# Kernel tuning notes

Measured on AMD Instinct MI355X. Metric: run time of the kernel, lower is better.

The kernel has to match this reference:

```python
import jax, jax.numpy as jnp
import numpy as np

K = 3   # spatial_kernel_size
M = 5   # memory_size


def setup_inputs() -> dict:
    key = jax.random.key(0)
    ks = jax.random.split(key, 16)
    C = 64
    B, H, D, W = 2, 24, 24, 24
    s = 0.05
    n = jax.random.normal
    return {
        "x": n(ks[0], (B, C, H, D, W), jnp.float32),
        "prev_memory": jnp.zeros((B, C), jnp.float32),
        "Wq": n(ks[1], (C, C), jnp.float32) * s,
        "bq": n(ks[2], (C,), jnp.float32) * s,
        "Wk": n(ks[3], (C, C), jnp.float32) * s,
        "bk": n(ks[4], (C,), jnp.float32) * s,
        "Wv": n(ks[5], (C, C), jnp.float32) * s,
        "bv": n(ks[6], (C,), jnp.float32) * s,
        "mem_key": n(ks[7], (C, M), jnp.float32),
        "mem_value": n(ks[8], (C, M), jnp.float32),
        "Wg": n(ks[9], (C, 2 * C), jnp.float32) * s,
        "bg": n(ks[10], (C,), jnp.float32) * s,
        "W_ih": n(ks[11], (3 * C, C), jnp.float32) * s,
        "W_hh": n(ks[12], (3 * C, C), jnp.float32) * s,
        "b_ih": n(ks[13], (3 * C,), jnp.float32) * s,
        "b_hh": n(ks[14], (3 * C,), jnp.float32) * s,
    }


def _patches(x, k):
    # x: (B,C,H,D,W) -> (B,C,k^3,H,D,W) local neighborhoods (zero-padded)
    B, C, H, D, W = x.shape
    p = k // 2
    xp = jnp.pad(x, ((0, 0), (0, 0), (p, p), (p, p), (p, p)))
    sl = [xp[:, :, i:i + H, j:j + D, l:l + W]
          for i in range(k) for j in range(k) for l in range(k)]
    return jnp.stack(sl, axis=2)


def reference(x, prev_memory, Wq, bq, Wk, bk, Wv, bv, mem_key, mem_value,
              Wg, bg, W_ih, W_hh, b_ih, b_hh):
    B, C, H, D, W = x.shape
    N = H * D * W
    xf = x.reshape(B, C, N)
    pf = _patches(x, K).reshape(B, C, K ** 3, N)

    # 1x1x1 conv projections (pure channel mixes)
    q = jnp.einsum('oc,bcn->bon', Wq, xf) + bq[None, :, None]            # (B,C,N)
    k_sp = jnp.einsum('oc,bcmn->bomn', Wk, pf) + bk[None, :, None, None]  # (B,C,27,N)
    v_sp = jnp.einsum('oc,bcmn->bomn', Wv, pf) + bv[None, :, None, None]

    # memory tokens broadcast over all spatial locations
    k_mem = jnp.broadcast_to(mem_key[None, :, :, None], (B, C, M, N))
    v_mem = jnp.broadcast_to(mem_value[None, :, :, None], (B, C, M, N))
    kk = jnp.concatenate([k_mem, k_sp], axis=2)   # (B,C,M+27,N)
    vv = jnp.concatenate([v_mem, v_sp], axis=2)

    # per-channel scalar attention over memory+neighborhood axis
    attn = jax.nn.softmax(q[:, :, None, :] * kk / jnp.sqrt(jnp.float32(C)), axis=2)
    out = jnp.sum(attn * vv, axis=2).reshape(B, C, H, D, W)

    # sigmoid gate over concat([x, out])
    gin = jnp.concatenate([xf, out.reshape(B, C, N)], axis=1)  # (B,2C,N)
    gate = jax.nn.sigmoid(jnp.einsum('oc,bcn->bon', Wg, gin)
                          + bg[None, :, None]).reshape(B, C, H, D, W)
    out = gate * out + (1.0 - gate) * x

    # GRU memory update on spatially pooled features (torch GRUCell math)
    mu = out.mean(axis=(2, 3, 4))                 # (B,C)
    gi = mu @ W_ih.T + b_ih
    gh = prev_memory @ W_hh.T + b_hh
    ir, iz, ii = jnp.split(gi, 3, axis=1)
    hr, hz, hn = jnp.split(gh, 3, axis=1)
    r = jax.nn.sigmoid(ir + hr)
    z = jax.nn.sigmoid(iz + hz)
    ng = jnp.tanh(ii + r * hn)
    new_memory = (1.0 - z) * ng + z * prev_memory
    return out, new_memory
```

## Files before the change

### kernel.cpp

```cpp
#include <hip/hip_runtime.h>
#include <math.h>

#define NPOS 13824
#define CDIM 64
#define BTCH 2
#define LOG2E 1.4426950408889634f

__global__ __launch_bounds__(256) void qkvg_kernel(
    const float* __restrict__ x,
    const float* __restrict__ Wq, const float* __restrict__ bq,
    const float* __restrict__ Wk, const float* __restrict__ bk,
    const float* __restrict__ Wv, const float* __restrict__ bv,
    const float* __restrict__ Wg,
    float* __restrict__ Qb, float* __restrict__ Kb, float* __restrict__ Vb,
    float* __restrict__ GXb, float* __restrict__ XT, float* __restrict__ pool)
{
  __shared__ __align__(16) float wqt[64*68];
  __shared__ __align__(16) float wkt[64*68];
  __shared__ __align__(16) float wvt[64*68];
  __shared__ __align__(16) float wgt[64*68];
  const int t  = threadIdx.x;
  const int bi = blockIdx.x;
  const int b  = bi / 216;
  const int n0 = (bi - b*216) * 64;
  if (bi == 0 && t < 128) pool[t] = 0.0f;

  #pragma unroll
  for (int k = 0; k < 16; ++k) {
    int idx = t + k*256;
    int lo = idx & 63, hi = idx >> 6;
    wqt[lo*68 + hi] = Wq[idx];
    wkt[lo*68 + hi] = Wk[idx];
    wvt[lo*68 + hi] = Wv[idx];
    wgt[lo*68 + hi] = Wg[hi*128 + lo];
  }
  __syncthreads();

  const int c0  = (t & 15) * 4;
  const int nn0 = (t >> 4) * 4;
  const float* xbase = x + (size_t)(b*64)*NPOS + n0 + nn0;
  float aq[4][4] = {}; float ak[4][4] = {}; float av[4][4] = {}; float ag[4][4] = {};
  #pragma unroll 4
  for (int cp = 0; cp < 64; ++cp) {
    const float4 xv4 = *(const float4*)(xbase + (size_t)cp*NPOS);
    const float4 q4  = *(const float4*)&wqt[cp*68 + c0];
    const float4 k4  = *(const float4*)&wkt[cp*68 + c0];
    const float4 v4  = *(const float4*)&wvt[cp*68 + c0];
    const float4 g4  = *(const float4*)&wgt[cp*68 + c0];
    const float xa[4] = {xv4.x, xv4.y, xv4.z, xv4.w};
    const float qa[4] = {q4.x, q4.y, q4.z, q4.w};
    const float ka[4] = {k4.x, k4.y, k4.z, k4.w};
    const float va[4] = {v4.x, v4.y, v4.z, v4.w};
    const float ga[4] = {g4.x, g4.y, g4.z, g4.w};
    #pragma unroll
    for (int ci = 0; ci < 4; ++ci)
      #pragma unroll
      for (int ni = 0; ni < 4; ++ni) {
        aq[ci][ni] = fmaf(qa[ci], xa[ni], aq[ci][ni]);
        ak[ci][ni] = fmaf(ka[ci], xa[ni], ak[ci][ni]);
        av[ci][ni] = fmaf(va[ci], xa[ni], av[ci][ni]);
        ag[ci][ni] = fmaf(ga[ci], xa[ni], ag[ci][ni]);
      }
  }
  const float4 bq4 = *(const float4*)&bq[c0];
  const float4 bk4 = *(const float4*)&bk[c0];
  const float4 bv4 = *(const float4*)&bv[c0];
  #pragma unroll
  for (int ni = 0; ni < 4; ++ni) {
    const int p = b*NPOS + n0 + nn0 + ni;
    float4 o;
    o = make_float4(aq[0][ni]+bq4.x, aq[1][ni]+bq4.y, aq[2][ni]+bq4.z, aq[3][ni]+bq4.w);
    *(float4*)&Qb[p*64 + c0] = o;
    o = make_float4(ak[0][ni]+bk4.x, ak[1][ni]+bk4.y, ak[2][ni]+bk4.z, ak[3][ni]+bk4.w);
    *(float4*)&Kb[p*64 + c0] = o;
    o = make_float4(av[0][ni]+bv4.x, av[1][ni]+bv4.y, av[2][ni]+bv4.z, av[3][ni]+bv4.w);
    *(float4*)&Vb[p*64 + c0] = o;
    o = make_float4(ag[0][ni], ag[1][ni], ag[2][ni], ag[3][ni]);
    *(float4*)&GXb[p*64 + c0] = o;
  }
  float4 xr[4];
  #pragma unroll
  for (int e = 0; e < 4; ++e)
    xr[e] = *(const float4*)(x + (size_t)(b*64 + c0 + e)*NPOS + n0 + nn0);
  const float xre[4][4] = {{xr[0].x,xr[0].y,xr[0].z,xr[0].w},
                           {xr[1].x,xr[1].y,xr[1].z,xr[1].w},
                           {xr[2].x,xr[2].y,xr[2].z,xr[2].w},
                           {xr[3].x,xr[3].y,xr[3].z,xr[3].w}};
  #pragma unroll
  for (int ni = 0; ni < 4; ++ni) {
    const int p = b*NPOS + n0 + nn0 + ni;
    *(float4*)&XT[p*64 + c0] = make_float4(xre[0][ni], xre[1][ni], xre[2][ni], xre[3][ni]);
  }
}

__global__ __launch_bounds__(256) void attn_kernel(
    float* __restrict__ QOT,
    const float* __restrict__ Kb, const float* __restrict__ Vb,
    const float* __restrict__ GXb, const float* __restrict__ XT,
    const float* __restrict__ bk, const float* __restrict__ bv,
    const float* __restrict__ memk, const float* __restrict__ memv,
    const float* __restrict__ Wg, const float* __restrict__ bg)
{
  __shared__ __align__(16) float smem[16000];
  __shared__ __align__(16) float als[256];
  const int t = threadIdx.x;
  const int c = t & 63;
  const int w = t >> 6;

  #pragma unroll
  for (int k = 0; k < 16; ++k) {
    int u = t + k*256;
    int cp = u >> 6, j = u & 63;
    smem[j*65 + cp] = Wg[cp*128 + 64 + j];
  }
  __syncthreads();
  float wg2reg[64];
  #pragma unroll
  for (int j = 0; j < 64; ++j) wg2reg[j] = smem[j*65 + c];
  float mk[5], mv[5];
  #pragma unroll
  for (int m = 0; m < 5; ++m) { mk[m] = memk[c*5 + m]; mv[m] = memv[c*5 + m]; }
  const float bg_c = bg[c];
  __syncthreads();

  const int bi = blockIdx.x;
  const int b  = bi >> 9;
  const int tb = bi & 511;
  const int h0 = (tb >> 6) * 3;
  const int d0 = ((tb >> 3) & 7) * 3;
  const int w0 = (tb & 7) * 3;
  const int bN = b * NPOS;

  for (int u = t; u < 125*16; u += 256) {
    int pos = u >> 4, q4 = u & 15;
    int ph = pos / 25, pr = pos - ph*25;
    int pd = pr / 5,  pw = pr - pd*5;
    int hh = h0 - 1 + ph, dd = d0 - 1 + pd, ww = w0 - 1 + pw;
    bool inb = ((unsigned)hh < 24u) && ((unsigned)dd < 24u) && ((unsigned)ww < 24u);
    float4 kf, vf;
    if (inb) {
      const size_t off = ((size_t)(bN + hh*576 + dd*24 + ww))*64 + q4*4;
      kf = *(const float4*)(Kb + off);
      vf = *(const float4*)(Vb + off);
    } else {
      kf = ((const float4*)bk)[q4];
      vf = ((const float4*)bv)[q4];
    }
    *(float4*)&smem[pos*64 + q4*4]        = kf;
    *(float4*)&smem[8000 + pos*64 + q4*4] = vf;
  }
  __syncthreads();

  for (int li = w; li < 27; li += 4) {
    const int lh = li / 9, lr = li - lh*9;
    const int ld = lr / 3, lw = lr - ld*3;
    const int p  = bN + (h0+lh)*576 + (d0+ld)*24 + (w0+lw);
    const int hb = (lh*25 + ld*5 + lw)*64 + c;

    const float q2 = QOT[p*64 + c] * (0.125f * LOG2E);
    float lg[32];
    #pragma unroll
    for (int m = 0; m < 5; ++m) lg[m] = q2 * mk[m];
    #pragma unroll
    for (int i = 0; i < 3; ++i)
      #pragma unroll
      for (int j = 0; j < 3; ++j)
        #pragma unroll
        for (int l = 0; l < 3; ++l)
          lg[5 + i*9 + j*3 + l] = q2 * smem[hb + (i*25 + j*5 + l)*64];

    float m0 = lg[0], m1 = lg[1], m2 = lg[2], m3 = lg[3];
    #pragma unroll
    for (int s4 = 4; s4 < 32; s4 += 4) {
      m0 = fmaxf(m0, lg[s4]);   m1 = fmaxf(m1, lg[s4+1]);
      m2 = fmaxf(m2, lg[s4+2]); m3 = fmaxf(m3, lg[s4+3]);
    }
    const float maxv = fmaxf(fmaxf(m0, m1), fmaxf(m2, m3));

    float s0 = 0.f, s1 = 0.f, o0 = 0.f, o1 = 0.f;
    #pragma unroll
    for (int m = 0; m < 5; ++m) {
      float pf = exp2f(lg[m] - maxv);
      if (m & 1) { s1 += pf; o1 = fmaf(pf, mv[m], o1); }
      else       { s0 += pf; o0 = fmaf(pf, mv[m], o0); }
    }
    #pragma unroll
    for (int i = 0; i < 3; ++i)
      #pragma unroll
      for (int j = 0; j < 3; ++j)
        #pragma unroll
        for (int l = 0; l < 3; ++l) {
          int s4 = i*9 + j*3 + l;
          float val = smem[8000 + hb + (i*25 + j*5 + l)*64];
          float pf = exp2f(lg[5 + s4] - maxv);
          if (s4 & 1) { s1 += pf; o1 = fmaf(pf, val, o1); }
          else        { s0 += pf; o0 = fmaf(pf, val, o0); }
        }
    const float att = (o0 + o1) * __builtin_amdgcn_rcpf(s0 + s1);

    als[w*64 + c] = att;
    float g0 = GXb[p*64 + c] + bg_c, g1 = 0.f, g2 = 0.f, g3 = 0.f;
    #pragma unroll
    for (int j4 = 0; j4 < 16; ++j4) {
      const float4 a4 = *(const float4*)&als[w*64 + j4*4];
      g0 = fmaf(wg2reg[j4*4+0], a4.x, g0);
      g1 = fmaf(wg2reg[j4*4+1], a4.y, g1);
      g2 = fmaf(wg2reg[j4*4+2], a4.z, g2);
      g3 = fmaf(wg2reg[j4*4+3], a4.w, g3);
    }
    const float gl   = (g0 + g1) + (g2 + g3);
    const float gate = __builtin_amdgcn_rcpf(1.0f + exp2f(-LOG2E * gl));
    const float xv   = XT[p*64 + c];
    QOT[p*64 + c] = fmaf(gate, att - xv, xv);
  }
}

__global__ __launch_bounds__(256) void outpool_kernel(
    const float* __restrict__ OT, float* __restrict__ out, float* __restrict__ pool)
{
  __shared__ __align__(16) float ls[64*65];
  const int t  = threadIdx.x;
  const int bi = blockIdx.x;
  const int b  = bi / 216;
  const int n0 = (bi - b*216) * 64;
  #pragma unroll
  for (int i = 0; i < 16; ++i) {
    int u = i*256 + t;
    int pos = u >> 6, cc = u & 63;
    ls[cc*65 + pos] = OT[(size_t)(b*NPOS + n0 + pos)*64 + cc];
  }
  __syncthreads();
  #pragma unroll
  for (int i = 0; i < 16; ++i) {
    int u = i*256 + t;
    int cc = u >> 6, j = u & 63;
    out[(size_t)(b*64 + cc)*NPOS + n0 + j] = ls[cc*65 + j];
  }
  if (t < 64) {
    float s = 0.0f;
    #pragma unroll 8
    for (int j = 0; j < 64; ++j) s += ls[t*65 + j];
    atomicAdd(&pool[b*64 + t], s);
  }
}

__global__ __launch_bounds__(384) void gru_kernel(
    const float* __restrict__ prev,
    const float* __restrict__ W_ih, const float* __restrict__ W_hh,
    const float* __restrict__ b_ih, const float* __restrict__ b_hh,
    const float* __restrict__ pool, float* __restrict__ outmem)
{
  __shared__ __align__(16) float mu[128];
  __shared__ float gi[384];
  __shared__ float gh[384];
  const int t = threadIdx.x;
  if (t < 128) mu[t] = pool[t] * (1.0f / (float)NPOS);
  __syncthreads();
  {
    int b = t / 192, j = t - b*192;
    const float4* wi4 = (const float4*)(W_ih + (size_t)j*64);
    const float4* wh4 = (const float4*)(W_hh + (size_t)j*64);
    const float4* mu4 = (const float4*)(mu + b*64);
    const float4* pv4 = (const float4*)(prev + b*64);
    float sgi = b_ih[j], sgh = b_hh[j];
    #pragma unroll
    for (int k = 0; k < 16; ++k) {
      float4 wv = wi4[k], m4 = mu4[k];
      sgi = fmaf(wv.x, m4.x, sgi); sgi = fmaf(wv.y, m4.y, sgi);
      sgi = fmaf(wv.z, m4.z, sgi); sgi = fmaf(wv.w, m4.w, sgi);
      float4 hv = wh4[k], p4 = pv4[k];
      sgh = fmaf(hv.x, p4.x, sgh); sgh = fmaf(hv.y, p4.y, sgh);
      sgh = fmaf(hv.z, p4.z, sgh); sgh = fmaf(hv.w, p4.w, sgh);
    }
    gi[t] = sgi; gh[t] = sgh;
  }
  __syncthreads();
  if (t < 128) {
    int b = t >> 6, cc = t & 63;
    float ir = gi[b*192 + cc],       hr = gh[b*192 + cc];
    float iz = gi[b*192 + 64 + cc],  hz = gh[b*192 + 64 + cc];
    float ii = gi[b*192 + 128 + cc], hn = gh[b*192 + 128 + cc];
    float rr = 1.0f / (1.0f + __expf(-(ir + hr)));
    float zz = 1.0f / (1.0f + __expf(-(iz + hz)));
    float ng = tanhf(ii + rr * hn);
    outmem[t] = (1.0f - zz) * ng + zz * prev[t];
  }
}

extern "C" void kernel_launch(void* const* d_in, const int* in_sizes, int n_in,
                              void* d_out, int out_size, void* d_ws, size_t ws_size,
                              hipStream_t stream) {
  const float* x    = (const float*)d_in[0];
  const float* prev = (const float*)d_in[1];
  const float* Wq   = (const float*)d_in[2];
  const float* bq   = (const float*)d_in[3];
  const float* Wk   = (const float*)d_in[4];
  const float* bk   = (const float*)d_in[5];
  const float* Wv   = (const float*)d_in[6];
  const float* bv   = (const float*)d_in[7];
  const float* memk = (const float*)d_in[8];
  const float* memv = (const float*)d_in[9];
  const float* Wg   = (const float*)d_in[10];
  const float* bg   = (const float*)d_in[11];
  const float* W_ih = (const float*)d_in[12];
  const float* W_hh = (const float*)d_in[13];
  const float* b_ih = (const float*)d_in[14];
  const float* b_hh = (const float*)d_in[15];

  float* out    = (float*)d_out;
  float* outmem = out + (size_t)BTCH*CDIM*NPOS;

  const size_t SZ = (size_t)BTCH*NPOS*CDIM;
  float* wsf  = (float*)d_ws;
  float* Qb   = wsf;
  float* Kb   = wsf + SZ;
  float* Vb   = wsf + 2*SZ;
  float* GXb  = wsf + 3*SZ;
  float* pool = wsf + 4*SZ;
  float* XT   = out;

  qkvg_kernel<<<BTCH*216, 256, 0, stream>>>(x, Wq, bq, Wk, bk, Wv, bv, Wg,
                                            Qb, Kb, Vb, GXb, XT, pool);
  attn_kernel<<<BTCH*512, 256, 0, stream>>>(Qb, Kb, Vb, GXb, XT,
                                            bk, bv, memk, memv, Wg, bg);
  outpool_kernel<<<BTCH*216, 256, 0, stream>>>(Qb, out, pool);
  gru_kernel<<<1, 384, 0, stream>>>(prev, W_ih, W_hh, b_ih, b_hh, pool, outmem);
}
```

Baseline: 162.1 us.

## Fuse output transpose, pooling and GRU update into attention kernel

The attention kernel now writes the gated output straight to the channel-major output from a shared-memory tile, reduces the pool sums per block, and uses a last-block-done counter so the final block runs the GRU update. This removes the separate outpool and GRU launches and the extra round trip of the output through the workspace. XT moves to a separate workspace buffer, and exp2f is replaced with the hardware exp2 builtin. In exchange, output stores become short strided runs of three elements, and the result depends on a global atomic counter being zeroed by the first kernel.

```diff
diff --git a/kernel.cpp b/kernel.cpp
--- a/kernel.cpp
+++ b/kernel.cpp
@@ -23,7 +23,7 @@
   const int bi = blockIdx.x;
   const int b  = bi / 216;
   const int n0 = (bi - b*216) * 64;
-  if (bi == 0 && t < 128) pool[t] = 0.0f;
+  if (bi == 0 && t < 132) pool[t] = 0.0f;
 
   #pragma unroll
   for (int k = 0; k < 16; ++k) {
@@ -93,19 +93,27 @@
   }
 }
 
-__global__ __launch_bounds__(256) void attn_kernel(
-    float* __restrict__ QOT,
+__global__ __launch_bounds__(256) void attn_fused(
+    const float* __restrict__ Qb,
     const float* __restrict__ Kb, const float* __restrict__ Vb,
     const float* __restrict__ GXb, const float* __restrict__ XT,
     const float* __restrict__ bk, const float* __restrict__ bv,
     const float* __restrict__ memk, const float* __restrict__ memv,
-    const float* __restrict__ Wg, const float* __restrict__ bg)
+    const float* __restrict__ Wg, const float* __restrict__ bg,
+    float* __restrict__ out, float* __restrict__ pool, int* __restrict__ cnt,
+    const float* __restrict__ prev,
+    const float* __restrict__ W_ih, const float* __restrict__ W_hh,
+    const float* __restrict__ b_ih, const float* __restrict__ b_hh,
+    float* __restrict__ outmem)
 {
   __shared__ __align__(16) float smem[16000];
+  __shared__ __align__(16) float fs[27*64];
   __shared__ __align__(16) float als[256];
+  __shared__ int flag;
   const int t = threadIdx.x;
   const int c = t & 63;
   const int w = t >> 6;
+  if (t == 0) flag = 0;
 
   #pragma unroll
   for (int k = 0; k < 16; ++k) {
@@ -151,13 +159,14 @@
   }
   __syncthreads();
 
+  float pacc = 0.0f;
   for (int li = w; li < 27; li += 4) {
     const int lh = li / 9, lr = li - lh*9;
     const int ld = lr / 3, lw = lr - ld*3;
     const int p  = bN + (h0+lh)*576 + (d0+ld)*24 + (w0+lw);
     const int hb = (lh*25 + ld*5 + lw)*64 + c;
 
-    const float q2 = QOT[p*64 + c] * (0.125f * LOG2E);
+    const float q2 = Qb[p*64 + c] * (0.125f * LOG2E);
     float lg[32];
     #pragma unroll
     for (int m = 0; m < 5; ++m) lg[m] = q2 * mk[m];
@@ -180,7 +189,7 @@
     float s0 = 0.f, s1 = 0.f, o0 = 0.f, o1 = 0.f;
     #pragma unroll
     for (int m = 0; m < 5; ++m) {
-      float pf = exp2f(lg[m] - maxv);
+      float pf = __builtin_amdgcn_exp2f(lg[m] - maxv);
       if (m & 1) { s1 += pf; o1 = fmaf(pf, mv[m], o1); }
       else       { s0 += pf; o0 = fmaf(pf, mv[m], o0); }
     }
@@ -192,7 +201,7 @@
         for (int l = 0; l < 3; ++l) {
           int s4 = i*9 + j*3 + l;
           float val = smem[8000 + hb + (i*25 + j*5 + l)*64];
-          float pf = exp2f(lg[5 + s4] - maxv);
+          float pf = __builtin_amdgcn_exp2f(lg[5 + s4] - maxv);
           if (s4 & 1) { s1 += pf; o1 = fmaf(pf, val, o1); }
           else        { s0 += pf; o0 = fmaf(pf, val, o0); }
         }
@@ -209,81 +218,71 @@
       g3 = fmaf(wg2reg[j4*4+3], a4.w, g3);
     }
     const float gl   = (g0 + g1) + (g2 + g3);
-    const float gate = __builtin_amdgcn_rcpf(1.0f + exp2f(-LOG2E * gl));
+    const float gate = __builtin_amdgcn_rcpf(1.0f + __builtin_amdgcn_exp2f(-LOG2E * gl));
     const float xv   = XT[p*64 + c];
-    QOT[p*64 + c] = fmaf(gate, att - xv, xv);
-  }
-}
-
-__global__ __launch_bounds__(256) void outpool_kernel(
-    const float* __restrict__ OT, float* __restrict__ out, float* __restrict__ pool)
-{
-  __shared__ __align__(16) float ls[64*65];
-  const int t  = threadIdx.x;
-  const int bi = blockIdx.x;
-  const int b  = bi / 216;
-  const int n0 = (bi - b*216) * 64;
-  #pragma unroll
-  for (int i = 0; i < 16; ++i) {
-    int u = i*256 + t;
-    int pos = u >> 6, cc = u & 63;
-    ls[cc*65 + pos] = OT[(size_t)(b*NPOS + n0 + pos)*64 + cc];
-  }
-  __syncthreads();
-  #pragma unroll
-  for (int i = 0; i < 16; ++i) {
-    int u = i*256 + t;
-    int cc = u >> 6, j = u & 63;
-    out[(size_t)(b*64 + cc)*NPOS + n0 + j] = ls[cc*65 + j];
-  }
+    const float fin  = fmaf(gate, att - xv, xv);
+    fs[li*64 + c] = fin;
+    pacc += fin;
+  }
+  __syncthreads();
+
+  for (int u = t; u < 576; u += 256) {
+    const int cc = u & 63, seg = u >> 6;
+    const int lh = seg / 3, ld = seg - lh*3;
+    const size_t o = (size_t)(b*64 + cc)*NPOS + (h0+lh)*576 + (d0+ld)*24 + w0;
+    const int f = (lh*9 + ld*3)*64 + cc;
+    out[o]     = fs[f];
+    out[o + 1] = fs[f + 64];
+    out[o + 2] = fs[f + 128];
+  }
+
+  als[t] = pacc;
+  __syncthreads();
   if (t < 64) {
-    float s = 0.0f;
-    #pragma unroll 8
-    for (int j = 0; j < 64; ++j) s += ls[t*65 + j];
+    float s = als[t] + als[64 + t] + als[128 + t] + als[192 + t];
     atomicAdd(&pool[b*64 + t], s);
   }
-}
-
-__global__ __launch_bounds__(384) void gru_kernel(
-    const float* __restrict__ prev,
-    const float* __restrict__ W_ih, const float* __restrict__ W_hh,
-    const float* __restrict__ b_ih, const float* __restrict__ b_hh,
-    const float* __restrict__ pool, float* __restrict__ outmem)
-{
-  __shared__ __align__(16) float mu[128];
-  __shared__ float gi[384];
-  __shared__ float gh[384];
-  const int t = threadIdx.x;
-  if (t < 128) mu[t] = pool[t] * (1.0f / (float)NPOS);
-  __syncthreads();
-  {
-    int b = t / 192, j = t - b*192;
-    const float4* wi4 = (const float4*)(W_ih + (size_t)j*64);
-    const float4* wh4 = (const float4*)(W_hh + (size_t)j*64);
-    const float4* mu4 = (const float4*)(mu + b*64);
-    const float4* pv4 = (const float4*)(prev + b*64);
-    float sgi = b_ih[j], sgh = b_hh[j];
-    #pragma unroll
-    for (int k = 0; k < 16; ++k) {
-      float4 wv = wi4[k], m4 = mu4[k];
-      sgi = fmaf(wv.x, m4.x, sgi); sgi = fmaf(wv.y, m4.y, sgi);
-      sgi = fmaf(wv.z, m4.z, sgi); sgi = fmaf(wv.w, m4.w, sgi);
-      float4 hv = wh4[k], p4 = pv4[k];
-      sgh = fmaf(hv.x, p4.x, sgh); sgh = fmaf(hv.y, p4.y, sgh);
-      sgh = fmaf(hv.z, p4.z, sgh); sgh = fmaf(hv.w, p4.w, sgh);
-    }
-    gi[t] = sgi; gh[t] = sgh;
-  }
-  __syncthreads();
-  if (t < 128) {
-    int b = t >> 6, cc = t & 63;
-    float ir = gi[b*192 + cc],       hr = gh[b*192 + cc];
-    float iz = gi[b*192 + 64 + cc],  hz = gh[b*192 + 64 + cc];
-    float ii = gi[b*192 + 128 + cc], hn = gh[b*192 + 128 + cc];
-    float rr = 1.0f / (1.0f + __expf(-(ir + hr)));
-    float zz = 1.0f / (1.0f + __expf(-(iz + hz)));
-    float ng = tanhf(ii + rr * hn);
-    outmem[t] = (1.0f - zz) * ng + zz * prev[t];
+  if (t == 0) {
+    __threadfence();
+    if (atomicAdd(cnt, 1) == (int)gridDim.x - 1) flag = 1;
+  }
+  __syncthreads();
+
+  if (flag) {
+    float* mu = fs; float* gi = fs + 128; float* gh = fs + 512;
+    if (t < 128)
+      mu[t] = __hip_atomic_load(&pool[t], __ATOMIC_RELAXED,
+                                __HIP_MEMORY_SCOPE_AGENT) * (1.0f / (float)NPOS);
+    __syncthreads();
+    for (int r = t; r < 384; r += 256) {
+      const int b2 = r / 192, j = r - b2*192;
+      const float4* wi4 = (const float4*)(W_ih + (size_t)j*64);
+      const float4* wh4 = (const float4*)(W_hh + (size_t)j*64);
+      const float4* mu4 = (const float4*)(mu + b2*64);
+      const float4* pv4 = (const float4*)(prev + b2*64);
+      float sgi = b_ih[j], sgh = b_hh[j];
+      #pragma unroll
+      for (int k = 0; k < 16; ++k) {
+        float4 wv = wi4[k], m4 = mu4[k];
+        sgi = fmaf(wv.x, m4.x, sgi); sgi = fmaf(wv.y, m4.y, sgi);
+        sgi = fmaf(wv.z, m4.z, sgi); sgi = fmaf(wv.w, m4.w, sgi);
+        float4 hv = wh4[k], p4 = pv4[k];
+        sgh = fmaf(hv.x, p4.x, sgh); sgh = fmaf(hv.y, p4.y, sgh);
+        sgh = fmaf(hv.z, p4.z, sgh); sgh = fmaf(hv.w, p4.w, sgh);
+      }
+      gi[r] = sgi; gh[r] = sgh;
+    }
+    __syncthreads();
+    if (t < 128) {
+      const int b2 = t >> 6, cc = t & 63;
+      float ir = gi[b2*192 + cc],       hr = gh[b2*192 + cc];
+      float iz = gi[b2*192 + 64 + cc],  hz = gh[b2*192 + 64 + cc];
+      float ii = gi[b2*192 + 128 + cc], hn = gh[b2*192 + 128 + cc];
+      float rr = 1.0f / (1.0f + __builtin_amdgcn_exp2f(-LOG2E * (ir + hr)));
+      float zz = 1.0f / (1.0f + __builtin_amdgcn_exp2f(-LOG2E * (iz + hz)));
+      float ng = tanhf(ii + rr * hn);
+      outmem[t] = (1.0f - zz) * ng + zz * prev[t];
+    }
   }
 }
 
@@ -316,13 +315,14 @@
   float* Kb   = wsf + SZ;
   float* Vb   = wsf + 2*SZ;
   float* GXb  = wsf + 3*SZ;
-  float* pool = wsf + 4*SZ;
-  float* XT   = out;
+  float* XT   = wsf + 4*SZ;
+  float* pool = wsf + 5*SZ;
+  int*   cnt  = (int*)(pool + 128);
 
   qkvg_kernel<<<BTCH*216, 256, 0, stream>>>(x, Wq, bq, Wk, bk, Wv, bv, Wg,
                                             Qb, Kb, Vb, GXb, XT, pool);
-  attn_kernel<<<BTCH*512, 256, 0, stream>>>(Qb, Kb, Vb, GXb, XT,
-                                            bk, bv, memk, memv, Wg, bg);
-  outpool_kernel<<<BTCH*216, 256, 0, stream>>>(Qb, out, pool);
-  gru_kernel<<<1, 384, 0, stream>>>(prev, W_ih, W_hh, b_ih, b_hh, pool, outmem);
+  attn_fused<<<BTCH*512, 256, 0, stream>>>(Qb, Kb, Vb, GXb, XT,
+                                           bk, bv, memk, memv, Wg, bg,
+                                           out, pool, cnt,
+                                           prev, W_ih, W_hh, b_ih, b_hh, outmem);
 }
```

Measured after the change: 187.2 us. 1.15x slower.
